# Optimization experiments

Hardware: AMD Instinct MI355X
Metric: run time of the kernel (lower is better)

The kernel has to match this reference:

```python
import jax, jax.numpy as jnp
import numpy as np
import math

NUM_HEADS = 16
SIZE = 1024
HEAD_SIZE = SIZE // NUM_HEADS
B, S = 2, 2048


def setup_inputs() -> dict:
    key = jax.random.key(0)
    ks = jax.random.split(key, 11)
    sc = 1.0 / math.sqrt(SIZE)
    inp = {
        "q": jax.random.normal(ks[0], (B, S, SIZE), dtype=jnp.float32),
        "k": jax.random.normal(ks[1], (B, S, SIZE), dtype=jnp.float32),
        "v": jax.random.normal(ks[2], (B, S, SIZE), dtype=jnp.float32),
        "Wq": jax.random.normal(ks[3], (SIZE, SIZE), dtype=jnp.float32) * sc,
        "bq": jax.random.normal(ks[4], (SIZE,), dtype=jnp.float32) * sc,
        "Wk": jax.random.normal(ks[5], (SIZE, SIZE), dtype=jnp.float32) * sc,
        "bk": jax.random.normal(ks[6], (SIZE,), dtype=jnp.float32) * sc,
        "Wv": jax.random.normal(ks[7], (SIZE, SIZE), dtype=jnp.float32) * sc,
        "bv": jax.random.normal(ks[8], (SIZE,), dtype=jnp.float32) * sc,
        "Wo": jax.random.normal(ks[9], (SIZE, SIZE), dtype=jnp.float32) * sc,
        "bo": jax.random.normal(ks[10], (SIZE,), dtype=jnp.float32) * sc,
    }
    return inp


def _split_heads(x):
    # [B, S, SIZE] -> [B, H, S, D]
    b, s, _ = x.shape
    return x.reshape(b, s, NUM_HEADS, HEAD_SIZE).transpose(0, 2, 1, 3)


def reference(q, k, v, Wq, bq, Wk, bk, Wv, bv, Wo, bo):
    qh = _split_heads(q @ Wq.T + bq) / math.sqrt(HEAD_SIZE)  # [B,H,S,D]
    kh = _split_heads(k @ Wk.T + bk)
    vh = _split_heads(v @ Wv.T + bv)
    scores = jnp.einsum("bhqd,bhkd->bhqk", qh, kh)  # [B,H,S,S]
    attn = jax.nn.softmax(scores, axis=-1)
    ctx = jnp.einsum("bhqk,bhkd->bhqd", attn, vh)  # [B,H,S,D]
    ctx = ctx.transpose(0, 2, 1, 3).reshape(q.shape[0], -1, SIZE)
    return ctx @ Wo.T + bo
```

## Files before the change

kernel.cpp:

```cpp
#include <hip/hip_runtime.h>
#include <hip/hip_bf16.h>

#define SIZE 1024
#define NH 16
#define HD 64
#define BB 2
#define SS 2048
#define MROWS (BB * SS)
#define QT 128
#define NQT (SS / QT)
#define NKT ((SS / 2) / 64)

using bf16 = __hip_bfloat16;
using frag16 = __attribute__((ext_vector_type(8))) short;
using f32x4 = __attribute__((ext_vector_type(4))) float;
typedef unsigned int u32;

__device__ __forceinline__ void glds16(const bf16* g, bf16* l) {
    __builtin_amdgcn_global_load_lds(
        (const __attribute__((address_space(1))) u32*)g,
        (__attribute__((address_space(3))) u32*)l, 16, 0, 0);
}

__device__ __forceinline__ void cvt_store8(bf16* dst, const float* src) {
    float4 a = *(const float4*)src;
    float4 b = *(const float4*)(src + 4);
    bf16 t[8];
    t[0] = __float2bfloat16(a.x); t[1] = __float2bfloat16(a.y);
    t[2] = __float2bfloat16(a.z); t[3] = __float2bfloat16(a.w);
    t[4] = __float2bfloat16(b.x); t[5] = __float2bfloat16(b.y);
    t[6] = __float2bfloat16(b.z); t[7] = __float2bfloat16(b.w);
    *(uint4*)dst = *(const uint4*)t;
}

__global__ __launch_bounds__(256) void cast_kernel(
    const float* __restrict__ Wq, const float* __restrict__ Wk,
    const float* __restrict__ Wv, const float* __restrict__ Wo,
    const float* __restrict__ q, const float* __restrict__ k,
    const float* __restrict__ v,
    bf16* __restrict__ Wb, bf16* __restrict__ qb,
    bf16* __restrict__ kb, bf16* __restrict__ vb)
{
    const int z = blockIdx.z;
    const float* s; bf16* d; int n;
    switch (z) {
        case 0: s = Wq; d = Wb;                   n = SIZE * SIZE;  break;
        case 1: s = Wk; d = Wb + SIZE * SIZE;     n = SIZE * SIZE;  break;
        case 2: s = Wv; d = Wb + 2 * SIZE * SIZE; n = SIZE * SIZE;  break;
        case 3: s = Wo; d = Wb + 3 * SIZE * SIZE; n = SIZE * SIZE;  break;
        case 4: s = q;  d = qb;                   n = MROWS * SIZE; break;
        case 5: s = k;  d = kb;                   n = MROWS * SIZE; break;
        default: s = v; d = vb;                   n = MROWS * SIZE; break;
    }
    const int i = (blockIdx.x * 256 + threadIdx.x) * 8;
    if (i < n) cvt_store8(d + i, s + i);
}

__device__ __forceinline__ void gemm_body(
    const bf16* __restrict__ X, const bf16* __restrict__ W,
    const float* __restrict__ bias, bf16* __restrict__ Y, float scale, bool vt_mode)
{
    __shared__ __align__(16) bf16 smem[8704];
    bf16* As = smem;
    bf16* Bs = smem + 4096;

    const int tid = threadIdx.x;
    const int wave = tid >> 6;
    const int lane = tid & 63;
    const int lane15 = lane & 15;
    const int quad = lane >> 4;
    const int bm = blockIdx.y * 128;
    const int bn = blockIdx.x * 128;
    const int wm = (wave & 1) * 64;
    const int wn = (wave >> 1) * 64;

    f32x4 acc[4][4];
#pragma unroll
    for (int i = 0; i < 4; i++)
#pragma unroll
        for (int j = 0; j < 4; j++)
            acc[i][j] = (f32x4){0.f, 0.f, 0.f, 0.f};

    const int srow = lane >> 2;
    const int scol = (lane & 3) * 8;

    for (int kt = 0; kt < SIZE / 32; kt++) {
        const int k0 = kt * 32;
        __syncthreads();
#pragma unroll
        for (int n = 0; n < 2; n++) {
            const int c = wave * 2 + n;
            glds16(X + (size_t)(bm + c * 16 + srow) * SIZE + k0 + scol, As + c * 512);
            glds16(W + (size_t)(bn + c * 16 + srow) * SIZE + k0 + scol, Bs + c * 512);
        }
        __syncthreads();

        frag16 a[4], b[4];
#pragma unroll
        for (int mi = 0; mi < 4; mi++)
            a[mi] = *(const frag16*)(As + (wm + mi * 16 + lane15) * 32 + quad * 8);
#pragma unroll
        for (int ni = 0; ni < 4; ni++)
            b[ni] = *(const frag16*)(Bs + (wn + ni * 16 + lane15) * 32 + quad * 8);
#pragma unroll
        for (int mi = 0; mi < 4; mi++)
#pragma unroll
            for (int ni = 0; ni < 4; ni++)
                acc[mi][ni] = __builtin_amdgcn_mfma_f32_16x16x32_bf16(
                    a[mi], b[ni], acc[mi][ni], 0, 0, 0);
    }

    if (!vt_mode) {
#pragma unroll
        for (int ni = 0; ni < 4; ni++) {
            const int col = bn + wn + ni * 16 + lane15;
            const float bv = bias[col];
#pragma unroll
            for (int mi = 0; mi < 4; mi++) {
                const int row = bm + wm + mi * 16 + quad * 4;
#pragma unroll
                for (int r = 0; r < 4; r++)
                    Y[(size_t)(row + r) * SIZE + col] =
                        __float2bfloat16((acc[mi][ni][r] + bv) * scale);
            }
        }
    } else {
        bf16* tr = smem;
        const int bloc = bm >> 11;
        const int s0g = bm & (SS - 1);
#pragma unroll
        for (int p = 0; p < 2; p++) {
            __syncthreads();
            if ((wave >> 1) == p) {
#pragma unroll
                for (int ni = 0; ni < 4; ni++) {
                    const int colp = ni * 16 + lane15;
                    const float bv = bias[bn + p * 64 + colp];
#pragma unroll
                    for (int mi = 0; mi < 4; mi++) {
                        const int row = wm + mi * 16 + quad * 4;
#pragma unroll
                        for (int r = 0; r < 4; r++)
                            tr[colp * 136 + row + r] =
                                __float2bfloat16(acc[mi][ni][r] + bv);
                    }
                }
            }
            __syncthreads();
            const int colp = tid >> 2;
            const int gcol = bn + p * 64 + colp;
            const int hh = gcol >> 6, dd = gcol & (HD - 1);
            bf16* dst = (bf16*)Y + ((size_t)(bloc * NH + hh) * HD + dd) * SS
                        + s0g + (tid & 3) * 32;
            const bf16* src = tr + colp * 136 + (tid & 3) * 32;
#pragma unroll
            for (int j = 0; j < 4; j++)
                *(uint4*)(dst + j * 8) = *(const uint4*)(src + j * 8);
        }
    }
}

__global__ __launch_bounds__(256) void qkv_proj_kernel(
    const bf16* __restrict__ qb, const bf16* __restrict__ kb, const bf16* __restrict__ vb,
    const bf16* __restrict__ Wb,
    const float* __restrict__ bq, const float* __restrict__ bk, const float* __restrict__ bv,
    bf16* __restrict__ qh, bf16* __restrict__ kh, bf16* __restrict__ vt)
{
    const bf16 *X, *W; const float* bi; bf16* Y; float sc; bool vm;
    if (blockIdx.z == 0)      { X = qb; W = Wb;                   bi = bq; Y = qh; sc = 0.125f; vm = false; }
    else if (blockIdx.z == 1) { X = kb; W = Wb + SIZE * SIZE;     bi = bk; Y = kh; sc = 1.0f;   vm = false; }
    else                      { X = vb; W = Wb + 2 * SIZE * SIZE; bi = bv; Y = vt; sc = 1.0f;   vm = true;  }
    gemm_body(X, W, bi, Y, sc, vm);
}

__global__ __launch_bounds__(256) void attn_kernel(
    const bf16* __restrict__ qh, const bf16* __restrict__ kh,
    const bf16* __restrict__ vt, bf16* __restrict__ po, float* __restrict__ pl)
{
    __shared__ __align__(16) bf16 Ks[64][72];
    __shared__ __align__(16) bf16 Vs[64][72];
    __shared__ __align__(16) bf16 Ps[4][32][72];

    const int tid = threadIdx.x;
    const int wave = tid >> 6;
    const int lane = tid & 63;
    const int lane15 = lane & 15;
    const int quad = lane >> 4;

    const int b = blockIdx.z, h = blockIdx.y;
    const int qt = blockIdx.x >> 1;
    const int sh = blockIdx.x & 1;
    const int q0 = qt * QT;

    const size_t baseq = (size_t)b * SS * SIZE + (size_t)h * HD;
    const size_t basev = (size_t)(b * NH + h) * HD * SS;
    const float LOG2E = 1.44269504088896340736f;
    const float OFF = 12.0f * LOG2E;

    frag16 aq[2][2];
#pragma unroll
    for (int m = 0; m < 2; m++) {
        const int qrow = q0 + wave * 32 + m * 16 + lane15;
        const bf16* qp = qh + baseq + (size_t)qrow * SIZE + quad * 8;
        aq[m][0] = *(const frag16*)(qp);
        aq[m][1] = *(const frag16*)(qp + 32);
    }

    frag16 bones;
#pragma unroll
    for (int e = 0; e < 8; e++) bones[e] = (short)0x3F80;

    f32x4 ofrag[2][4], l_frag[2];
#pragma unroll
    for (int m = 0; m < 2; m++) {
        l_frag[m] = (f32x4){0.f, 0.f, 0.f, 0.f};
#pragma unroll
        for (int dt = 0; dt < 4; dt++) ofrag[m][dt] = (f32x4){0.f, 0.f, 0.f, 0.f};
    }

    const int sr = tid >> 3;
    const int sc = (tid & 7) * 8;

    for (int kt = 0; kt < NKT; kt++) {
        const int s0 = sh * (SS / 2) + kt * 64;
        __syncthreads();
        *(uint4*)&Ks[sr][sc]      = *(const uint4*)(kh + baseq + (size_t)(s0 + sr) * SIZE + sc);
        *(uint4*)&Ks[sr + 32][sc] = *(const uint4*)(kh + baseq + (size_t)(s0 + sr + 32) * SIZE + sc);
        *(uint4*)&Vs[sr][sc]      = *(const uint4*)(vt + basev + (size_t)sr * SS + s0 + sc);
        *(uint4*)&Vs[sr + 32][sc] = *(const uint4*)(vt + basev + (size_t)(sr + 32) * SS + s0 + sc);
        __syncthreads();

        frag16 kf[4][2];
#pragma unroll
        for (int nt = 0; nt < 4; nt++) {
            kf[nt][0] = *(const frag16*)&Ks[nt * 16 + lane15][quad * 8];
            kf[nt][1] = *(const frag16*)&Ks[nt * 16 + lane15][32 + quad * 8];
        }
#pragma unroll
        for (int m = 0; m < 2; m++) {
#pragma unroll
            for (int nt = 0; nt < 4; nt++) {
                f32x4 c = (f32x4){0.f, 0.f, 0.f, 0.f};
                c = __builtin_amdgcn_mfma_f32_16x16x32_bf16(kf[nt][0], aq[m][0], c, 0, 0, 0);
                c = __builtin_amdgcn_mfma_f32_16x16x32_bf16(kf[nt][1], aq[m][1], c, 0, 0, 0);
                bf16 p4[4];
#pragma unroll
                for (int r = 0; r < 4; r++)
                    p4[r] = __float2bfloat16(exp2f(fminf(c[r], 30.f) * LOG2E - OFF));
                *(uint2*)&Ps[wave][m * 16 + lane15][nt * 16 + quad * 4] = *(const uint2*)p4;
            }
        }
        __builtin_amdgcn_wave_barrier();

        frag16 ap[2][2];
#pragma unroll
        for (int m = 0; m < 2; m++)
#pragma unroll
            for (int c2 = 0; c2 < 2; c2++)
                ap[m][c2] = *(const frag16*)&Ps[wave][m * 16 + lane15][c2 * 32 + quad * 8];

#pragma unroll
        for (int m = 0; m < 2; m++)
#pragma unroll
            for (int c2 = 0; c2 < 2; c2++)
                l_frag[m] = __builtin_amdgcn_mfma_f32_16x16x32_bf16(
                    ap[m][c2], bones, l_frag[m], 0, 0, 0);

#pragma unroll
        for (int dt = 0; dt < 4; dt++) {
            frag16 bv0 = *(const frag16*)&Vs[dt * 16 + lane15][quad * 8];
            frag16 bv1 = *(const frag16*)&Vs[dt * 16 + lane15][32 + quad * 8];
#pragma unroll
            for (int m = 0; m < 2; m++) {
                ofrag[m][dt] = __builtin_amdgcn_mfma_f32_16x16x32_bf16(ap[m][0], bv0, ofrag[m][dt], 0, 0, 0);
                ofrag[m][dt] = __builtin_amdgcn_mfma_f32_16x16x32_bf16(ap[m][1], bv1, ofrag[m][dt], 0, 0, 0);
            }
        }
    }

    const int pb = ((b * NH + h) * NQT + qt) * 2 + sh;
    if (lane15 == 0) {
        float* plp = pl + (size_t)pb * QT;
#pragma unroll
        for (int m = 0; m < 2; m++)
#pragma unroll
            for (int r = 0; r < 4; r++)
                plp[wave * 32 + m * 16 + quad * 4 + r] = l_frag[m][r];
    }
    bf16* pop = po + (size_t)pb * QT * HD;
#pragma unroll
    for (int m = 0; m < 2; m++)
#pragma unroll
        for (int dt = 0; dt < 4; dt++)
#pragma unroll
            for (int r = 0; r < 4; r++)
                pop[(size_t)(wave * 32 + m * 16 + quad * 4 + r) * HD + dt * 16 + lane15] =
                    __float2bfloat16(ofrag[m][dt][r]);
}

__global__ __launch_bounds__(256) void combine_kernel(
    const bf16* __restrict__ po, const float* __restrict__ pl, bf16* __restrict__ ctx)
{
    const int b = blockIdx.z, h = blockIdx.y, qt = blockIdx.x;
    const int tile = (b * NH + h) * NQT + qt;
    const bf16* p0 = po + (size_t)(tile * 2 + 0) * QT * HD;
    const bf16* p1 = po + (size_t)(tile * 2 + 1) * QT * HD;
    const int qr = threadIdx.x >> 1;
    const int dh = (threadIdx.x & 1) * 32;
    const float l = pl[(size_t)(tile * 2) * QT + qr] + pl[(size_t)(tile * 2 + 1) * QT + qr];
    const float inv = 1.0f / fmaxf(l, 1e-30f);
    bf16* dst = ctx + ((size_t)b * SS + qt * QT + qr) * SIZE + h * HD + dh;
    const bf16* s0p = p0 + qr * HD + dh;
    const bf16* s1p = p1 + qr * HD + dh;
#pragma unroll
    for (int j = 0; j < 32; j += 8) {
        uint4 u0 = *(const uint4*)(s0p + j);
        uint4 u1 = *(const uint4*)(s1p + j);
        const bf16* a = (const bf16*)&u0;
        const bf16* bt = (const bf16*)&u1;
        bf16 o[8];
#pragma unroll
        for (int e = 0; e < 8; e++)
            o[e] = __float2bfloat16((__bfloat162float(a[e]) + __bfloat162float(bt[e])) * inv);
        *(uint4*)(dst + j) = *(const uint4*)o;
    }
}

__global__ __launch_bounds__(256) void out_proj_kernel(
    const bf16* __restrict__ ctx, const bf16* __restrict__ Wob,
    const float* __restrict__ bo, float* __restrict__ out)
{
    __shared__ __align__(16) bf16 As[64 * 32];
    __shared__ __align__(16) bf16 Bs[128 * 32];

    const int tid = threadIdx.x;
    const int wave = tid >> 6;
    const int lane = tid & 63;
    const int lane15 = lane & 15;
    const int quad = lane >> 4;
    const int bm = blockIdx.y * 64;
    const int bn = blockIdx.x * 128;
    const int wn = wave * 32;

    f32x4 acc[4][2];
#pragma unroll
    for (int i = 0; i < 4; i++)
#pragma unroll
        for (int j = 0; j < 2; j++)
            acc[i][j] = (f32x4){0.f, 0.f, 0.f, 0.f};

    const int srow = lane >> 2;
    const int scol = (lane & 3) * 8;

    for (int kt = 0; kt < SIZE / 32; kt++) {
        const int k0 = kt * 32;
        __syncthreads();
        glds16(ctx + (size_t)(bm + wave * 16 + srow) * SIZE + k0 + scol, As + wave * 512);
#pragma unroll
        for (int n = 0; n < 2; n++) {
            const int c = wave * 2 + n;
            glds16(Wob + (size_t)(bn + c * 16 + srow) * SIZE + k0 + scol, Bs + c * 512);
        }
        __syncthreads();

        frag16 a[4], b[2];
#pragma unroll
        for (int mi = 0; mi < 4; mi++)
            a[mi] = *(const frag16*)(As + (mi * 16 + lane15) * 32 + quad * 8);
#pragma unroll
        for (int ni = 0; ni < 2; ni++)
            b[ni] = *(const frag16*)(Bs + (wn + ni * 16 + lane15) * 32 + quad * 8);
#pragma unroll
        for (int mi = 0; mi < 4; mi++)
#pragma unroll
            for (int ni = 0; ni < 2; ni++)
                acc[mi][ni] = __builtin_amdgcn_mfma_f32_16x16x32_bf16(
                    a[mi], b[ni], acc[mi][ni], 0, 0, 0);
    }

#pragma unroll
    for (int ni = 0; ni < 2; ni++) {
        const int col = bn + wn + ni * 16 + lane15;
        const float bv = bo[col];
#pragma unroll
        for (int mi = 0; mi < 4; mi++) {
            const int row = bm + mi * 16 + quad * 4;
#pragma unroll
            for (int r = 0; r < 4; r++)
                out[(size_t)(row + r) * SIZE + col] = acc[mi][ni][r] + bv;
        }
    }
}

extern "C" void kernel_launch(void* const* d_in, const int* in_sizes, int n_in,
                              void* d_out, int out_size, void* d_ws, size_t ws_size,
                              hipStream_t stream) {
    const float* q  = (const float*)d_in[0];
    const float* k  = (const float*)d_in[1];
    const float* v  = (const float*)d_in[2];
    const float* Wq = (const float*)d_in[3];
    const float* bq = (const float*)d_in[4];
    const float* Wk = (const float*)d_in[5];
    const float* bk = (const float*)d_in[6];
    const float* Wv = (const float*)d_in[7];
    const float* bv = (const float*)d_in[8];
    const float* Wo = (const float*)d_in[9];
    const float* bo = (const float*)d_in[10];
    float* out = (float*)d_out;

    bf16* Wb  = (bf16*)d_ws;
    bf16* qb  = Wb + (size_t)4 * SIZE * SIZE;
    bf16* kb  = qb + (size_t)MROWS * SIZE;
    bf16* vb  = kb + (size_t)MROWS * SIZE;
    bf16* qh  = vb + (size_t)MROWS * SIZE;
    bf16* kh  = qh + (size_t)MROWS * SIZE;
    bf16* vt  = kh + (size_t)MROWS * SIZE;
    bf16* po  = qb;
    bf16* ctx = vb;
    float* pl = (float*)Wb;

    cast_kernel<<<dim3(MROWS * SIZE / 2048, 1, 7), 256, 0, stream>>>(
        Wq, Wk, Wv, Wo, q, k, v, Wb, qb, kb, vb);
    qkv_proj_kernel<<<dim3(SIZE / 128, MROWS / 128, 3), 256, 0, stream>>>(
        qb, kb, vb, Wb, bq, bk, bv, qh, kh, vt);
    attn_kernel<<<dim3(NQT * 2, NH, BB), 256, 0, stream>>>(qh, kh, vt, po, pl);
    combine_kernel<<<dim3(NQT, NH, BB), 256, 0, stream>>>(po, pl, ctx);
    out_proj_kernel<<<dim3(SIZE / 128, MROWS / 64, 1), 256, 0, stream>>>(
        ctx, Wb + (size_t)3 * SIZE * SIZE, bo, out);
}
```

Measured before the change: 261.2 us.

## Fuse activation cast into QKV GEMM, merge combine into out-proj, double-buffer attention

Drops the separate fp32-to-bf16 cast of q/k/v: the QKV GEMM now loads fp32 rows and converts them into LDS itself, so only the weights are pre-cast. The split-KV combine kernel is removed, and the out-projection reads both partial outputs and their row sums, normalises them and stages the result as its A operand. The attention loop moves to 32-key tiles with double-buffered async global-to-LDS loads and XOR-swizzled LDS layouts. The cost is fp32 reads re-converted by every column block of the QKV GEMM, and the combine work redone by every N-block of the out-projection.

```diff
diff --git a/kernel.cpp b/kernel.cpp
--- a/kernel.cpp
+++ b/kernel.cpp
@@ -9,7 +9,8 @@
 #define MROWS (BB * SS)
 #define QT 128
 #define NQT (SS / QT)
-#define NKT ((SS / 2) / 64)
+#define KT32 32
+#define NKT2 ((SS / 2) / KT32)
 
 using bf16 = __hip_bfloat16;
 using frag16 = __attribute__((ext_vector_type(8))) short;
@@ -33,36 +34,32 @@
     *(uint4*)dst = *(const uint4*)t;
 }
 
-__global__ __launch_bounds__(256) void cast_kernel(
+__global__ __launch_bounds__(256) void cast_w_kernel(
     const float* __restrict__ Wq, const float* __restrict__ Wk,
     const float* __restrict__ Wv, const float* __restrict__ Wo,
-    const float* __restrict__ q, const float* __restrict__ k,
-    const float* __restrict__ v,
-    bf16* __restrict__ Wb, bf16* __restrict__ qb,
-    bf16* __restrict__ kb, bf16* __restrict__ vb)
+    bf16* __restrict__ Wb)
 {
-    const int z = blockIdx.z;
-    const float* s; bf16* d; int n;
-    switch (z) {
-        case 0: s = Wq; d = Wb;                   n = SIZE * SIZE;  break;
-        case 1: s = Wk; d = Wb + SIZE * SIZE;     n = SIZE * SIZE;  break;
-        case 2: s = Wv; d = Wb + 2 * SIZE * SIZE; n = SIZE * SIZE;  break;
-        case 3: s = Wo; d = Wb + 3 * SIZE * SIZE; n = SIZE * SIZE;  break;
-        case 4: s = q;  d = qb;                   n = MROWS * SIZE; break;
-        case 5: s = k;  d = kb;                   n = MROWS * SIZE; break;
-        default: s = v; d = vb;                   n = MROWS * SIZE; break;
-    }
+    const float* srcs[4] = {Wq, Wk, Wv, Wo};
+    const float* s = srcs[blockIdx.z];
+    bf16* d = Wb + (size_t)blockIdx.z * SIZE * SIZE;
     const int i = (blockIdx.x * 256 + threadIdx.x) * 8;
-    if (i < n) cvt_store8(d + i, s + i);
-}
-
-__device__ __forceinline__ void gemm_body(
-    const bf16* __restrict__ X, const bf16* __restrict__ W,
-    const float* __restrict__ bias, bf16* __restrict__ Y, float scale, bool vt_mode)
+    cvt_store8(d + i, s + i);
+}
+
+__global__ __launch_bounds__(256) void qkv_proj_kernel(
+    const float* __restrict__ q, const float* __restrict__ k, const float* __restrict__ v,
+    const bf16* __restrict__ Wb,
+    const float* __restrict__ bq, const float* __restrict__ bk, const float* __restrict__ bv,
+    bf16* __restrict__ qh, bf16* __restrict__ kh, bf16* __restrict__ vt)
 {
     __shared__ __align__(16) bf16 smem[8704];
     bf16* As = smem;
     bf16* Bs = smem + 4096;
+
+    const float *X, *bi; const bf16* W; bf16* Y; float scale; bool vm;
+    if (blockIdx.z == 0)      { X = q; W = Wb;                   bi = bq; Y = qh; scale = 0.125f; vm = false; }
+    else if (blockIdx.z == 1) { X = k; W = Wb + SIZE * SIZE;     bi = bk; Y = kh; scale = 1.0f;   vm = false; }
+    else                      { X = v; W = Wb + 2 * SIZE * SIZE; bi = bv; Y = vt; scale = 1.0f;   vm = true;  }
 
     const int tid = threadIdx.x;
     const int wave = tid >> 6;
@@ -81,18 +78,25 @@
         for (int j = 0; j < 4; j++)
             acc[i][j] = (f32x4){0.f, 0.f, 0.f, 0.f};
 
+    const int r0 = tid >> 2, c0 = (tid & 3) * 8, r1 = r0 + 64;
+    const float* xp0 = X + (size_t)(bm + r0) * SIZE + c0;
+    const float* xp1 = X + (size_t)(bm + r1) * SIZE + c0;
     const int srow = lane >> 2;
     const int scol = (lane & 3) * 8;
 
     for (int kt = 0; kt < SIZE / 32; kt++) {
         const int k0 = kt * 32;
         __syncthreads();
+        float4 fa0[2], fa1[2];
+        fa0[0] = *(const float4*)(xp0 + k0); fa0[1] = *(const float4*)(xp0 + k0 + 4);
+        fa1[0] = *(const float4*)(xp1 + k0); fa1[1] = *(const float4*)(xp1 + k0 + 4);
 #pragma unroll
         for (int n = 0; n < 2; n++) {
             const int c = wave * 2 + n;
-            glds16(X + (size_t)(bm + c * 16 + srow) * SIZE + k0 + scol, As + c * 512);
             glds16(W + (size_t)(bn + c * 16 + srow) * SIZE + k0 + scol, Bs + c * 512);
         }
+        cvt_store8(As + r0 * 32 + c0, (const float*)fa0);
+        cvt_store8(As + r1 * 32 + c0, (const float*)fa1);
         __syncthreads();
 
         frag16 a[4], b[4];
@@ -110,11 +114,11 @@
                     a[mi], b[ni], acc[mi][ni], 0, 0, 0);
     }
 
-    if (!vt_mode) {
+    if (!vm) {
 #pragma unroll
         for (int ni = 0; ni < 4; ni++) {
             const int col = bn + wn + ni * 16 + lane15;
-            const float bv = bias[col];
+            const float bv = bi[col];
 #pragma unroll
             for (int mi = 0; mi < 4; mi++) {
                 const int row = bm + wm + mi * 16 + quad * 4;
@@ -135,7 +139,7 @@
 #pragma unroll
                 for (int ni = 0; ni < 4; ni++) {
                     const int colp = ni * 16 + lane15;
-                    const float bv = bias[bn + p * 64 + colp];
+                    const float bv = bi[bn + p * 64 + colp];
 #pragma unroll
                     for (int mi = 0; mi < 4; mi++) {
                         const int row = wm + mi * 16 + quad * 4;
@@ -160,26 +164,13 @@
     }
 }
 
-__global__ __launch_bounds__(256) void qkv_proj_kernel(
-    const bf16* __restrict__ qb, const bf16* __restrict__ kb, const bf16* __restrict__ vb,
-    const bf16* __restrict__ Wb,
-    const float* __restrict__ bq, const float* __restrict__ bk, const float* __restrict__ bv,
-    bf16* __restrict__ qh, bf16* __restrict__ kh, bf16* __restrict__ vt)
-{
-    const bf16 *X, *W; const float* bi; bf16* Y; float sc; bool vm;
-    if (blockIdx.z == 0)      { X = qb; W = Wb;                   bi = bq; Y = qh; sc = 0.125f; vm = false; }
-    else if (blockIdx.z == 1) { X = kb; W = Wb + SIZE * SIZE;     bi = bk; Y = kh; sc = 1.0f;   vm = false; }
-    else                      { X = vb; W = Wb + 2 * SIZE * SIZE; bi = bv; Y = vt; sc = 1.0f;   vm = true;  }
-    gemm_body(X, W, bi, Y, sc, vm);
-}
-
 __global__ __launch_bounds__(256) void attn_kernel(
     const bf16* __restrict__ qh, const bf16* __restrict__ kh,
     const bf16* __restrict__ vt, bf16* __restrict__ po, float* __restrict__ pl)
 {
-    __shared__ __align__(16) bf16 Ks[64][72];
-    __shared__ __align__(16) bf16 Vs[64][72];
-    __shared__ __align__(16) bf16 Ps[4][32][72];
+    __shared__ __align__(16) bf16 Ks[2][KT32 * 64];
+    __shared__ __align__(16) bf16 Vs[2][64 * KT32];
+    __shared__ __align__(16) bf16 Ps[4][32 * 40];
 
     const int tid = threadIdx.x;
     const int wave = tid >> 6;
@@ -218,28 +209,43 @@
         for (int dt = 0; dt < 4; dt++) ofrag[m][dt] = (f32x4){0.f, 0.f, 0.f, 0.f};
     }
 
-    const int sr = tid >> 3;
-    const int sc = (tid & 7) * 8;
-
-    for (int kt = 0; kt < NKT; kt++) {
-        const int s0 = sh * (SS / 2) + kt * 64;
-        __syncthreads();
-        *(uint4*)&Ks[sr][sc]      = *(const uint4*)(kh + baseq + (size_t)(s0 + sr) * SIZE + sc);
-        *(uint4*)&Ks[sr + 32][sc] = *(const uint4*)(kh + baseq + (size_t)(s0 + sr + 32) * SIZE + sc);
-        *(uint4*)&Vs[sr][sc]      = *(const uint4*)(vt + basev + (size_t)sr * SS + s0 + sc);
-        *(uint4*)&Vs[sr + 32][sc] = *(const uint4*)(vt + basev + (size_t)(sr + 32) * SS + s0 + sc);
-        __syncthreads();
-
-        frag16 kf[4][2];
-#pragma unroll
-        for (int nt = 0; nt < 4; nt++) {
-            kf[nt][0] = *(const frag16*)&Ks[nt * 16 + lane15][quad * 8];
-            kf[nt][1] = *(const frag16*)&Ks[nt * 16 + lane15][32 + quad * 8];
-        }
+    const int krow = wave * 8 + (lane >> 3);
+    const int kgl  = ((lane & 7) ^ ((lane >> 3) & 7)) * 8;
+    const int vrow = wave * 16 + (lane >> 2);
+    const int vgl  = ((lane & 3) ^ ((lane >> 2) & 3)) * 8;
+    const int s00 = sh * (SS / 2);
+
+#define STAGE(BUF, KT)                                                          \
+    {                                                                           \
+        const int s0_ = s00 + (KT) * KT32;                                      \
+        glds16(kh + baseq + (size_t)(s0_ + krow) * SIZE + kgl,                  \
+               &Ks[BUF][wave * 512]);                                           \
+        glds16(vt + basev + (size_t)vrow * SS + s0_ + vgl,                      \
+               &Vs[BUF][wave * 512]);                                           \
+    }
+
+    STAGE(0, 0);
+    __syncthreads();
+
+    for (int kt = 0; kt < NKT2; kt++) {
+        const int cur = kt & 1;
+        if (kt + 1 < NKT2) STAGE(cur ^ 1, kt + 1);
+
+        frag16 kf[2][2];
+#pragma unroll
+        for (int nt = 0; nt < 2; nt++) {
+            const int row = nt * 16 + lane15;
+#pragma unroll
+            for (int c2 = 0; c2 < 2; c2++) {
+                const int pg = (c2 * 4 + quad) ^ (row & 7);
+                kf[nt][c2] = *(const frag16*)(&Ks[cur][0] + row * 64 + pg * 8);
+            }
+        }
+
 #pragma unroll
         for (int m = 0; m < 2; m++) {
 #pragma unroll
-            for (int nt = 0; nt < 4; nt++) {
+            for (int nt = 0; nt < 2; nt++) {
                 f32x4 c = (f32x4){0.f, 0.f, 0.f, 0.f};
                 c = __builtin_amdgcn_mfma_f32_16x16x32_bf16(kf[nt][0], aq[m][0], c, 0, 0, 0);
                 c = __builtin_amdgcn_mfma_f32_16x16x32_bf16(kf[nt][1], aq[m][1], c, 0, 0, 0);
@@ -247,36 +253,34 @@
 #pragma unroll
                 for (int r = 0; r < 4; r++)
                     p4[r] = __float2bfloat16(exp2f(fminf(c[r], 30.f) * LOG2E - OFF));
-                *(uint2*)&Ps[wave][m * 16 + lane15][nt * 16 + quad * 4] = *(const uint2*)p4;
+                *(uint2*)(&Ps[wave][0] + (m * 16 + lane15) * 40 + nt * 16 + quad * 4) =
+                    *(const uint2*)p4;
             }
         }
         __builtin_amdgcn_wave_barrier();
 
-        frag16 ap[2][2];
+        frag16 ap[2];
 #pragma unroll
         for (int m = 0; m < 2; m++)
-#pragma unroll
-            for (int c2 = 0; c2 < 2; c2++)
-                ap[m][c2] = *(const frag16*)&Ps[wave][m * 16 + lane15][c2 * 32 + quad * 8];
+            ap[m] = *(const frag16*)(&Ps[wave][0] + (m * 16 + lane15) * 40 + quad * 8);
 
 #pragma unroll
         for (int m = 0; m < 2; m++)
-#pragma unroll
-            for (int c2 = 0; c2 < 2; c2++)
-                l_frag[m] = __builtin_amdgcn_mfma_f32_16x16x32_bf16(
-                    ap[m][c2], bones, l_frag[m], 0, 0, 0);
+            l_frag[m] = __builtin_amdgcn_mfma_f32_16x16x32_bf16(ap[m], bones, l_frag[m], 0, 0, 0);
 
 #pragma unroll
         for (int dt = 0; dt < 4; dt++) {
-            frag16 bv0 = *(const frag16*)&Vs[dt * 16 + lane15][quad * 8];
-            frag16 bv1 = *(const frag16*)&Vs[dt * 16 + lane15][32 + quad * 8];
-#pragma unroll
-            for (int m = 0; m < 2; m++) {
-                ofrag[m][dt] = __builtin_amdgcn_mfma_f32_16x16x32_bf16(ap[m][0], bv0, ofrag[m][dt], 0, 0, 0);
-                ofrag[m][dt] = __builtin_amdgcn_mfma_f32_16x16x32_bf16(ap[m][1], bv1, ofrag[m][dt], 0, 0, 0);
-            }
-        }
-    }
+            const int row = dt * 16 + lane15;
+            const int pg = quad ^ (row & 3);
+            frag16 bv = *(const frag16*)(&Vs[cur][0] + row * 32 + pg * 8);
+#pragma unroll
+            for (int m = 0; m < 2; m++)
+                ofrag[m][dt] = __builtin_amdgcn_mfma_f32_16x16x32_bf16(ap[m], bv, ofrag[m][dt], 0, 0, 0);
+        }
+
+        __syncthreads();
+    }
+#undef STAGE
 
     const int pb = ((b * NH + h) * NQT + qt) * 2 + sh;
     if (lane15 == 0) {
@@ -298,37 +302,10 @@
                     __float2bfloat16(ofrag[m][dt][r]);
 }
 
-__global__ __launch_bounds__(256) void combine_kernel(
-    const bf16* __restrict__ po, const float* __restrict__ pl, bf16* __restrict__ ctx)
-{
-    const int b = blockIdx.z, h = blockIdx.y, qt = blockIdx.x;
-    const int tile = (b * NH + h) * NQT + qt;
-    const bf16* p0 = po + (size_t)(tile * 2 + 0) * QT * HD;
-    const bf16* p1 = po + (size_t)(tile * 2 + 1) * QT * HD;
-    const int qr = threadIdx.x >> 1;
-    const int dh = (threadIdx.x & 1) * 32;
-    const float l = pl[(size_t)(tile * 2) * QT + qr] + pl[(size_t)(tile * 2 + 1) * QT + qr];
-    const float inv = 1.0f / fmaxf(l, 1e-30f);
-    bf16* dst = ctx + ((size_t)b * SS + qt * QT + qr) * SIZE + h * HD + dh;
-    const bf16* s0p = p0 + qr * HD + dh;
-    const bf16* s1p = p1 + qr * HD + dh;
-#pragma unroll
-    for (int j = 0; j < 32; j += 8) {
-        uint4 u0 = *(const uint4*)(s0p + j);
-        uint4 u1 = *(const uint4*)(s1p + j);
-        const bf16* a = (const bf16*)&u0;
-        const bf16* bt = (const bf16*)&u1;
-        bf16 o[8];
-#pragma unroll
-        for (int e = 0; e < 8; e++)
-            o[e] = __float2bfloat16((__bfloat162float(a[e]) + __bfloat162float(bt[e])) * inv);
-        *(uint4*)(dst + j) = *(const uint4*)o;
-    }
-}
-
 __global__ __launch_bounds__(256) void out_proj_kernel(
-    const bf16* __restrict__ ctx, const bf16* __restrict__ Wob,
-    const float* __restrict__ bo, float* __restrict__ out)
+    const bf16* __restrict__ po, const float* __restrict__ pl,
+    const bf16* __restrict__ Wob, const float* __restrict__ bo,
+    float* __restrict__ out)
 {
     __shared__ __align__(16) bf16 As[64 * 32];
     __shared__ __align__(16) bf16 Bs[128 * 32];
@@ -349,13 +326,33 @@
         for (int j = 0; j < 2; j++)
             acc[i][j] = (f32x4){0.f, 0.f, 0.f, 0.f};
 
-    const int srow = lane >> 2;
-    const int scol = (lane & 3) * 8;
+    const int ar = tid >> 2, ac = (tid & 3) * 8;
+    const int gm = bm + ar;
+    const int bb = gm >> 11, s = gm & (SS - 1);
+    const int qtile = s >> 7, qr = s & (QT - 1);
+    const int tbase = (bb * NH) * NQT + qtile;
+    const int srow = lane >> 2, scol = (lane & 3) * 8;
 
     for (int kt = 0; kt < SIZE / 32; kt++) {
         const int k0 = kt * 32;
         __syncthreads();
-        glds16(ctx + (size_t)(bm + wave * 16 + srow) * SIZE + k0 + scol, As + wave * 512);
+        {
+            const int hh = k0 >> 6;
+            const size_t tile = (size_t)(tbase + hh * NQT) * 2;
+            const int d = (k0 & 32) + ac;
+            uint4 u0 = *(const uint4*)(po + ((tile + 0) * QT + qr) * HD + d);
+            uint4 u1 = *(const uint4*)(po + ((tile + 1) * QT + qr) * HD + d);
+            const float l = pl[(tile + 0) * QT + qr] + pl[(tile + 1) * QT + qr];
+            const float inv = 1.0f / fmaxf(l, 1e-30f);
+            const bf16* a0 = (const bf16*)&u0;
+            const bf16* a1 = (const bf16*)&u1;
+            bf16 t[8];
+#pragma unroll
+            for (int e = 0; e < 8; e++)
+                t[e] = __float2bfloat16(
+                    (__bfloat162float(a0[e]) + __bfloat162float(a1[e])) * inv);
+            *(uint4*)(As + ar * 32 + ac) = *(const uint4*)t;
+        }
 #pragma unroll
         for (int n = 0; n < 2; n++) {
             const int c = wave * 2 + n;
@@ -408,23 +405,18 @@
     const float* bo = (const float*)d_in[10];
     float* out = (float*)d_out;
 
-    bf16* Wb  = (bf16*)d_ws;
-    bf16* qb  = Wb + (size_t)4 * SIZE * SIZE;
-    bf16* kb  = qb + (size_t)MROWS * SIZE;
-    bf16* vb  = kb + (size_t)MROWS * SIZE;
-    bf16* qh  = vb + (size_t)MROWS * SIZE;
-    bf16* kh  = qh + (size_t)MROWS * SIZE;
-    bf16* vt  = kh + (size_t)MROWS * SIZE;
-    bf16* po  = qb;
-    bf16* ctx = vb;
-    float* pl = (float*)Wb;
-
-    cast_kernel<<<dim3(MROWS * SIZE / 2048, 1, 7), 256, 0, stream>>>(
-        Wq, Wk, Wv, Wo, q, k, v, Wb, qb, kb, vb);
+    bf16* Wb = (bf16*)d_ws;
+    bf16* qh = Wb + (size_t)4 * SIZE * SIZE;
+    bf16* kh = qh + (size_t)MROWS * SIZE;
+    bf16* vt = kh + (size_t)MROWS * SIZE;
+    bf16* po = vt + (size_t)MROWS * SIZE;
+    float* pl = (float*)(po + (size_t)1024 * QT * HD);
+
+    cast_w_kernel<<<dim3(SIZE * SIZE / 2048, 1, 4), 256, 0, stream>>>(
+        Wq, Wk, Wv, Wo, Wb);
     qkv_proj_kernel<<<dim3(SIZE / 128, MROWS / 128, 3), 256, 0, stream>>>(
-        qb, kb, vb, Wb, bq, bk, bv, qh, kh, vt);
+        q, k, v, Wb, bq, bk, bv, qh, kh, vt);
     attn_kernel<<<dim3(NQT * 2, NH, BB), 256, 0, stream>>>(qh, kh, vt, po, pl);
-    combine_kernel<<<dim3(NQT, NH, BB), 256, 0, stream>>>(po, pl, ctx);
     out_proj_kernel<<<dim3(SIZE / 128, MROWS / 64, 1), 256, 0, stream>>>(
-        ctx, Wb + (size_t)3 * SIZE * SIZE, bo, out);
-}
+        po, pl, Wb + (size_t)3 * SIZE * SIZE, bo, out);
+}
```

Measured after the change: 297.2 us. +13.8%, slower.
